# Optimization experiments

Hardware: AMD Instinct MI355X
Metric: run time of the kernel (lower is better)

The kernel has to match this reference:

```python
import jax, jax.numpy as jnp
import numpy as np

NEG_SLOPE = 0.2


def setup_inputs() -> dict:
    key = jax.random.key(0)
    ks = jax.random.split(key, 6)
    N, E, IN, H, D = 50000, 800000, 256, 4, 64
    x = jax.random.normal(ks[0], (N, IN), dtype=jnp.float32)
    edge_index = jax.random.randint(ks[1], (2, E), 0, N, dtype=jnp.int64)
    W = jax.random.normal(ks[2], (IN, H * D), dtype=jnp.float32) / np.sqrt(IN)
    att_src = jax.random.normal(ks[3], (H, D), dtype=jnp.float32) / np.sqrt(D)
    att_dst = jax.random.normal(ks[4], (H, D), dtype=jnp.float32) / np.sqrt(D)
    bias = jnp.zeros((H * D,), dtype=jnp.float32)
    return {"x": x, "edge_index": edge_index, "W": W,
            "att_src": att_src, "att_dst": att_dst, "bias": bias}


def reference(x, edge_index, W, att_src, att_dst, bias):
    N = x.shape[0]
    H, D = att_src.shape
    # add self-loops (PyG GATConv default add_self_loops=True)
    loops = jnp.arange(N, dtype=edge_index.dtype)
    src = jnp.concatenate([edge_index[0], loops])  # [E']
    dst = jnp.concatenate([edge_index[1], loops])  # [E']
    # per-head linear transform: [N, H, D]
    h = (x @ W).reshape(N, H, D)
    # per-node attention logits per head: [N, H]
    a_s = jnp.einsum('nhd,hd->nh', h, att_src)
    a_d = jnp.einsum('nhd,hd->nh', h, att_dst)
    # per-edge raw attention: [E', H]
    e = jax.nn.leaky_relu(a_s[src] + a_d[dst], NEG_SLOPE)
    # softmax over edges grouped by destination node (stable)
    m = jax.ops.segment_max(e, dst, num_segments=N)
    e = jnp.exp(e - m[dst])
    s = jax.ops.segment_sum(e, dst, num_segments=N)
    alpha = e / s[dst]  # every node has a self-loop -> s > 0
    # weighted scatter-aggregate: [N, H, D]
    out = jax.ops.segment_sum(alpha[:, :, None] * h[src], dst, num_segments=N)
    # concat heads + bias; dropout=0.0 -> identity
    return out.reshape(N, H * D) + bias
```

## Files before the change

kernel.cpp:

```cpp
#include <hip/hip_runtime.h>
#include <hip/hip_bf16.h>

#define NEG_SLOPE 0.2f
#define HPAD 264

typedef short short8 __attribute__((ext_vector_type(8)));
typedef float floatx4 __attribute__((ext_vector_type(4)));
typedef unsigned short ushort8v __attribute__((ext_vector_type(8)));
typedef unsigned short ushort4v __attribute__((ext_vector_type(4)));
typedef unsigned int uint4v __attribute__((ext_vector_type(4)));

__device__ __forceinline__ float bf2f_raw(unsigned short u) {
    union { float f; unsigned u; } c; c.u = ((unsigned)u) << 16; return c.f;
}
__device__ __forceinline__ float asf(unsigned u) {
    union { float f; unsigned u; } c; c.u = u; return c.f;
}
__device__ __forceinline__ unsigned short f2bf_raw(float f) {
    union { float f; unsigned u; } c; c.f = f;
    unsigned u = c.u;
    u += 0x7FFFu + ((u >> 16) & 1u);
    return (unsigned short)(u >> 16);
}
__device__ __forceinline__ float ldf(const void* p, size_t i, int f32) {
    return f32 ? ((const float*)p)[i] : bf2f_raw(((const unsigned short*)p)[i]);
}
__device__ __forceinline__ unsigned short ldbf(const void* p, size_t i, int f32) {
    return f32 ? f2bf_raw(((const float*)p)[i]) : ((const unsigned short*)p)[i];
}
__device__ __forceinline__ int clampN(long long v, int N) {
    if (v < 0) v = 0;
    if (v >= N) v = N - 1;
    return (int)v;
}
__device__ __forceinline__ float lrelu(float v) { return v > 0.f ? v : NEG_SLOPE * v; }

__global__ __launch_bounds__(256) void prep_kernel(
    const void* __restrict__ W, unsigned short* __restrict__ Wt,
    const unsigned short* __restrict__ x,
    const unsigned short* __restrict__ as_, const unsigned short* __restrict__ ad_,
    const unsigned* __restrict__ edge_w, int* __restrict__ flags, int edge_words,
    int* __restrict__ deg8, int* __restrict__ bsync, int N8)
{
    __shared__ float sm[256];
    __shared__ unsigned su[256];
    const int t = threadIdx.x;
    const int i = blockIdx.x * 256 + t;

    #pragma unroll
    for (int j = 0; j < 7; ++j) {
        int z = i + j * 65536;
        if (z < N8) deg8[z] = 0;
    }
    if (i < 256) bsync[i] = 0;

    float mw = 0.f;
    for (int k = t; k < 4096; k += 256) {
        float v = fabsf(bf2f_raw(((const unsigned short*)W)[k]));
        mw = fmaxf(mw, (v == v && v < 3e38f) ? v : 1e9f);
    }
    sm[t] = mw; __syncthreads();
    for (int s = 128; s; s >>= 1) { if (t < s) sm[t] = fmaxf(sm[t], sm[t + s]); __syncthreads(); }
    const int wf32 = sm[0] > 100.f;
    __syncthreads();

    if (blockIdx.x == 0) {
        float mx = 0.f, ma = 0.f;
        for (int k = t; k < 4096; k += 256) {
            float v = fabsf(bf2f_raw(x[k]));
            mx = fmaxf(mx, (v == v && v < 3e38f) ? v : 1e9f);
        }
        {
            float v1 = fabsf(bf2f_raw(as_[t]));
            float v2 = fabsf(bf2f_raw(ad_[t]));
            v1 = (v1 == v1 && v1 < 3e38f) ? v1 : 1e9f;
            v2 = (v2 == v2 && v2 < 3e38f) ? v2 : 1e9f;
            ma = fmaxf(v1, v2);
        }
        unsigned ow = 0;
        {
            int k = 2 * t + 1;
            if (k < edge_words) ow = edge_w[k];
        }
        sm[t] = mx; __syncthreads();
        for (int s = 128; s; s >>= 1) { if (t < s) sm[t] = fmaxf(sm[t], sm[t + s]); __syncthreads(); }
        if (t == 0) flags[0] = sm[0] > 100.f;
        __syncthreads();
        sm[t] = ma; __syncthreads();
        for (int s = 128; s; s >>= 1) { if (t < s) sm[t] = fmaxf(sm[t], sm[t + s]); __syncthreads(); }
        if (t == 0) flags[2] = sm[0] > 100.f;
        __syncthreads();
        su[t] = ow; __syncthreads();
        for (int s = 128; s; s >>= 1) { if (t < s) su[t] |= su[t + s]; __syncthreads(); }
        if (t == 0) { flags[3] = (su[0] == 0u); flags[1] = wf32; }
    }

    int j = i & 7;
    int l = (i >> 3) & 63;
    int ks = (i >> 9) & 7;
    int c = i >> 12;
    int k = ks * 32 + (l >> 4) * 8 + j;
    int n = c * 16 + (l & 15);
    Wt[i] = ldbf(W, (size_t)k * 256 + n, wf32);
}

__global__ __launch_bounds__(512) void gemm_count_kernel(
    const void* __restrict__ x, const unsigned short* __restrict__ Wt,
    const void* __restrict__ att_src, const void* __restrict__ att_dst,
    unsigned short* __restrict__ h_out, float* __restrict__ a_s, float* __restrict__ a_d,
    const void* __restrict__ edge, int* __restrict__ deg8, int* __restrict__ rank,
    const int* __restrict__ flags, int N, int E, int ntiles,
    int ngemm, int ncount, int ntotal)
{
    const unsigned long long bi = blockIdx.x;
    const unsigned before = (unsigned)((bi * (unsigned long long)ncount) / ntotal);
    const unsigned after  = (unsigned)(((bi + 1) * (unsigned long long)ncount) / ntotal);

    if (after != before) {
        const int cb = (int)before;
        const int base = cb * 2048 + threadIdx.x * 4;
        if (base >= E) return;
        int* my = deg8 + (size_t)(cb & 7) * N;
        const int cnt = (E - base < 4) ? (E - base) : 4;
        int d[4];
        if (flags[3]) {
            const long long* p = (const long long*)edge + E + base;
            #pragma unroll
            for (int k = 0; k < 4; ++k) d[k] = clampN((k < cnt) ? p[k] : 0, N);
        } else {
            const int* p = (const int*)edge + E + base;
            #pragma unroll
            for (int k = 0; k < 4; ++k) d[k] = clampN((k < cnt) ? (long long)p[k] : 0, N);
        }
        int r[4] = {0, 0, 0, 0};
        #pragma unroll
        for (int k = 0; k < 4; ++k)
            if (k < cnt) r[k] = atomicAdd(&my[d[k]], 1);
        #pragma unroll
        for (int k = 0; k < 4; ++k)
            if (k < cnt) rank[base + k] = r[k];
        return;
    }

    const int gb = (int)(bi - before);

    __shared__ unsigned short sh_h[32][HPAD];
    __shared__ float sh_a[2][32][4];

    const int w = threadIdx.x >> 6;
    const int head = w >> 1;
    const int st = w & 1;
    const int l = threadIdx.x & 63;
    const int lane16 = l & 15;
    const int quad = l >> 4;
    const int xf = flags[0], af = flags[2];
    const int n0w = head * 64;

    float as_att[4], ad_att[4];
    #pragma unroll
    for (int nt = 0; nt < 4; ++nt) {
        as_att[nt] = ldf(att_src, n0w + nt * 16 + lane16, af);
        ad_att[nt] = ldf(att_dst, n0w + nt * 16 + lane16, af);
    }

    for (int tile = gb; tile < ntiles; tile += ngemm) {
        const int m0 = tile * 32;
        int r0 = m0 + st * 16 + lane16;
        if (r0 >= N) r0 = N - 1;

        floatx4 acc[4];
        #pragma unroll
        for (int nt = 0; nt < 4; ++nt) acc[nt] = (floatx4){0.f, 0.f, 0.f, 0.f};

        const unsigned short* wp0 = Wt + (((size_t)head * 32) * 64 + l) * 8;

        #pragma unroll
        for (int half = 0; half < 2; ++half) {
            short8 fa[4];
            if (!xf) {
                const char* b0 = (const char*)x + ((size_t)r0 * 256 + quad * 8) * 2 + half * 256;
                #pragma unroll
                for (int k4 = 0; k4 < 4; ++k4)
                    fa[k4] = *(const short8*)(b0 + k4 * 64);
            } else {
                const float* b0 = (const float*)x + (size_t)r0 * 256 + quad * 8 + half * 128;
                #pragma unroll
                for (int k4 = 0; k4 < 4; ++k4) {
                    #pragma unroll
                    for (int j = 0; j < 8; ++j)
                        fa[k4][j] = (short)f2bf_raw(b0[k4 * 32 + j]);
                }
            }

            #pragma unroll
            for (int k4 = 0; k4 < 4; ++k4) {
                const unsigned short* wp = wp0 + (size_t)(half * 4 + k4) * 512;
                #pragma unroll
                for (int nt = 0; nt < 4; ++nt) {
                    short8 fb = *(const short8*)(wp + nt * 4096);
                    acc[nt] = __builtin_amdgcn_mfma_f32_16x16x32_bf16(fa[k4], fb, acc[nt], 0, 0, 0);
                }
            }
        }

        __syncthreads();

        #pragma unroll
        for (int nt = 0; nt < 4; ++nt) {
            #pragma unroll
            for (int r = 0; r < 4; ++r) {
                sh_h[st * 16 + quad * 4 + r][n0w + nt * 16 + lane16] = f2bf_raw(acc[nt][r]);
            }
        }
        #pragma unroll
        for (int r = 0; r < 4; ++r) {
            float vs = acc[0][r] * as_att[0] + acc[1][r] * as_att[1]
                     + acc[2][r] * as_att[2] + acc[3][r] * as_att[3];
            float vd = acc[0][r] * ad_att[0] + acc[1][r] * ad_att[1]
                     + acc[2][r] * ad_att[2] + acc[3][r] * ad_att[3];
            vs += __shfl_xor(vs, 1); vs += __shfl_xor(vs, 2);
            vs += __shfl_xor(vs, 4); vs += __shfl_xor(vs, 8);
            vd += __shfl_xor(vd, 1); vd += __shfl_xor(vd, 2);
            vd += __shfl_xor(vd, 4); vd += __shfl_xor(vd, 8);
            if (lane16 == 0) {
                const int row = st * 16 + quad * 4 + r;
                sh_a[0][row][head] = vs;
                sh_a[1][row][head] = vd;
            }
        }

        __syncthreads();

        #pragma unroll
        for (int p = 0; p < 2; ++p) {
            const int c = p * 512 + threadIdx.x;
            const int row = c >> 5;
            const int ch = c & 31;
            if (m0 + row < N) {
                ushort8v v = *(const ushort8v*)&sh_h[row][ch * 8];
                *(ushort8v*)(h_out + (size_t)(m0 + row) * 256 + ch * 8) = v;
            }
        }
        {
            const int t = threadIdx.x;
            if (t < 32) {
                if (m0 + t < N)
                    *(floatx4*)&a_s[(size_t)(m0 + t) * 4] = *(const floatx4*)&sh_a[0][t][0];
            } else if (t >= 64 && t < 96) {
                const int r = t - 64;
                if (m0 + r < N)
                    *(floatx4*)&a_d[(size_t)(m0 + r) * 4] = *(const floatx4*)&sh_a[1][r][0];
            }
        }
    }
}

__global__ __launch_bounds__(256) void scan_fused_kernel(
    const int* __restrict__ deg8, int* __restrict__ deg,
    int* __restrict__ row_off, int* __restrict__ cursor8,
    int* __restrict__ bsum, int* __restrict__ bbase, int* __restrict__ bsync,
    int N, int nb)
{
    __shared__ int sh[256];
    __shared__ int is_last;
    __shared__ int sbase;
    const int b = blockIdx.x, t = threadIdx.x;
    const int base_i = b * 1024 + t * 4;
    int v[4], ts = 0;
    #pragma unroll
    for (int i = 0; i < 4; ++i) {
        int idx = base_i + i;
        int tot = 0;
        if (idx < N) {
            #pragma unroll
            for (int x = 0; x < 8; ++x) tot += deg8[(size_t)x * N + idx];
        }
        v[i] = tot;
        ts += tot;
    }
    sh[t] = ts; __syncthreads();
    for (int off = 1; off < 256; off <<= 1) {
        int add = (t >= off) ? sh[t - off] : 0;
        __syncthreads();
        sh[t] += add;
        __syncthreads();
    }
    if (t == 255) {
        __hip_atomic_store(&bsum[b], sh[255], __ATOMIC_RELEASE, __HIP_MEMORY_SCOPE_AGENT);
        int arrived = __hip_atomic_fetch_add(&bsync[0], 1, __ATOMIC_ACQ_REL, __HIP_MEMORY_SCOPE_AGENT);
        is_last = (arrived == nb - 1);
    }
    __syncthreads();
    if (is_last) {
        if (nb <= 64) {
            if (t < 64) {
                int val = (t < nb)
                    ? __hip_atomic_load(&bsum[t], __ATOMIC_ACQUIRE, __HIP_MEMORY_SCOPE_AGENT) : 0;
                int incl = val;
                #pragma unroll
                for (int off = 1; off < 64; off <<= 1) {
                    int u = __shfl_up(incl, off);
                    if (t >= off) incl += u;
                }
                if (t < nb)
                    __hip_atomic_store(&bbase[t], incl - val, __ATOMIC_RELEASE, __HIP_MEMORY_SCOPE_AGENT);
            }
        } else if (t == 0) {
            int run = 0;
            for (int i = 0; i < nb; ++i) {
                int s = __hip_atomic_load(&bsum[i], __ATOMIC_ACQUIRE, __HIP_MEMORY_SCOPE_AGENT);
                __hip_atomic_store(&bbase[i], run, __ATOMIC_RELEASE, __HIP_MEMORY_SCOPE_AGENT);
                run += s;
            }
        }
        __syncthreads();
        if (t == 0)
            __hip_atomic_store(&bsync[1], 1, __ATOMIC_RELEASE, __HIP_MEMORY_SCOPE_AGENT);
    }
    if (t == 0) {
        while (__hip_atomic_load(&bsync[1], __ATOMIC_ACQUIRE, __HIP_MEMORY_SCOPE_AGENT) == 0) {}
        sbase = __hip_atomic_load(&bbase[b], __ATOMIC_RELAXED, __HIP_MEMORY_SCOPE_AGENT);
    }
    __syncthreads();
    int run = sbase + sh[t] - ts;
    #pragma unroll
    for (int i = 0; i < 4; ++i) {
        int idx = base_i + i;
        if (idx < N) {
            row_off[idx] = run;
            deg[idx] = v[i];
            int c = run;
            #pragma unroll
            for (int x = 0; x < 8; ++x) {
                cursor8[(size_t)x * N + idx] = c;
                c += deg8[(size_t)x * N + idx];
            }
        }
        run += v[i];
    }
}

__global__ __launch_bounds__(512) void scatter_kernel(
    const void* __restrict__ edge, const int* __restrict__ cursor8,
    const int* __restrict__ rank, int* __restrict__ elist,
    const int* __restrict__ flags, int E, int N)
{
    const int base = blockIdx.x * 2048 + threadIdx.x * 4;
    if (base >= E) return;
    const int* mybase = cursor8 + (size_t)(blockIdx.x & 7) * N;
    const int cnt = (E - base < 4) ? (E - base) : 4;
    int s[4], d[4];
    if (flags[3]) {
        const long long* ps = (const long long*)edge + base;
        const long long* pd = (const long long*)edge + E + base;
        #pragma unroll
        for (int k = 0; k < 4; ++k) {
            s[k] = clampN((k < cnt) ? ps[k] : 0, N);
            d[k] = clampN((k < cnt) ? pd[k] : 0, N);
        }
    } else {
        const int* ps = (const int*)edge + base;
        const int* pd = (const int*)edge + E + base;
        #pragma unroll
        for (int k = 0; k < 4; ++k) {
            s[k] = clampN((k < cnt) ? (long long)ps[k] : 0, N);
            d[k] = clampN((k < cnt) ? (long long)pd[k] : 0, N);
        }
    }
    #pragma unroll
    for (int k = 0; k < 4; ++k) {
        if (k < cnt) {
            int pos = mybase[d[k]] + rank[base + k];
            elist[pos] = s[k];
        }
    }
}

__global__ __launch_bounds__(256) void aggregate_kernel(
    const int* __restrict__ row_off, const int* __restrict__ deg,
    const int* __restrict__ elist,
    const float* __restrict__ a_s, const float* __restrict__ a_d,
    const unsigned short* __restrict__ h_ws,
    const void* __restrict__ bias, void* __restrict__ out,
    const int* __restrict__ flags, int N)
{
    const int n = blockIdx.x * 4 + (threadIdx.x >> 6);
    if (n >= N) return;
    const int lane = threadIdx.x & 63;
    const int q = lane >> 4;
    const int li = lane & 15;
    const int head = li >> 2;
    const int col0 = li * 16;

    const int dn = deg[n];
    const int row = row_off[n];
    const float adn = a_d[n * 4 + head];
    const float self_logit = lrelu(a_s[n * 4 + head] + adn);

    float acc[16];
    {
        const uint4v* hp = (const uint4v*)(h_ws + (size_t)n * 256 + col0);
        uint4v ha = hp[0], hb = hp[1];
        #pragma unroll
        for (int w = 0; w < 4; ++w) {
            acc[2 * w]         = (q == 0) ? asf(ha[w] << 16) : 0.f;
            acc[2 * w + 1]     = (q == 0) ? asf(ha[w] & 0xffff0000u) : 0.f;
            acc[8 + 2 * w]     = (q == 0) ? asf(hb[w] << 16) : 0.f;
            acc[8 + 2 * w + 1] = (q == 0) ? asf(hb[w] & 0xffff0000u) : 0.f;
        }
    }
    float ssum = (q == 0) ? 1.f : 0.f;

    float asA, asB;
    uint4v hA0, hA1, hB0, hB1;
    int sC, sD;
    {
        int e0 = q, e1 = 4 + q, e2 = 8 + q, e3 = 12 + q;
        int s0 = (e0 < dn) ? elist[row + e0] : n;
        int s1 = (e1 < dn) ? elist[row + e1] : n;
        sC = (e2 < dn) ? elist[row + e2] : n;
        sD = (e3 < dn) ? elist[row + e3] : n;
        asA = a_s[s0 * 4 + head];
        asB = a_s[s1 * 4 + head];
        const uint4v* pA = (const uint4v*)(h_ws + (size_t)s0 * 256 + col0);
        const uint4v* pB = (const uint4v*)(h_ws + (size_t)s1 * 256 + col0);
        hA0 = pA[0]; hA1 = pA[1];
        hB0 = pB[0]; hB1 = pB[1];
    }

    for (int c0 = 0; c0 < dn; c0 += 8) {
        {
            float p = __expf(lrelu(asA + adn) - self_logit);
            p = (c0 + q < dn) ? p : 0.f;
            ssum += p;
            #pragma unroll
            for (int w = 0; w < 4; ++w) {
                acc[2 * w]         += p * asf(hA0[w] << 16);
                acc[2 * w + 1]     += p * asf(hA0[w] & 0xffff0000u);
                acc[8 + 2 * w]     += p * asf(hA1[w] << 16);
                acc[8 + 2 * w + 1] += p * asf(hA1[w] & 0xffff0000u);
            }
        }
        {
            asA = a_s[sC * 4 + head];
            const uint4v* p = (const uint4v*)(h_ws + (size_t)sC * 256 + col0);
            hA0 = p[0]; hA1 = p[1];
            int e = c0 + 16 + q;
            sC = (e < dn) ? elist[row + e] : n;
        }
        {
            float p = __expf(lrelu(asB + adn) - self_logit);
            p = (c0 + 4 + q < dn) ? p : 0.f;
            ssum += p;
            #pragma unroll
            for (int w = 0; w < 4; ++w) {
                acc[2 * w]         += p * asf(hB0[w] << 16);
                acc[2 * w + 1]     += p * asf(hB0[w] & 0xffff0000u);
                acc[8 + 2 * w]     += p * asf(hB1[w] << 16);
                acc[8 + 2 * w + 1] += p * asf(hB1[w] & 0xffff0000u);
            }
        }
        {
            asB = a_s[sD * 4 + head];
            const uint4v* p = (const uint4v*)(h_ws + (size_t)sD * 256 + col0);
            hB0 = p[0]; hB1 = p[1];
            int e = c0 + 20 + q;
            sD = (e < dn) ? elist[row + e] : n;
        }
    }

    #pragma unroll
    for (int j = 0; j < 16; ++j) {
        acc[j] += __shfl_xor(acc[j], 16);
        acc[j] += __shfl_xor(acc[j], 32);
    }
    float stot = ssum + __shfl_xor(ssum, 16);
    stot += __shfl_xor(stot, 32);

    const float inv = 1.f / stot;
    const int j0 = q * 4;
    const int bf32 = flags[2];
    float o[4];
    #pragma unroll
    for (int k = 0; k < 4; ++k)
        o[k] = acc[j0 + k] * inv + ldf(bias, col0 + j0 + k, bf32);
    if (flags[0]) {
        float* op = (float*)out + (size_t)n * 256 + col0 + j0;
        __builtin_nontemporal_store((floatx4){o[0], o[1], o[2], o[3]}, (floatx4*)op);
    } else {
        ushort4v ov;
        #pragma unroll
        for (int k = 0; k < 4; ++k) ov[k] = f2bf_raw(o[k]);
        __builtin_nontemporal_store(ov,
            (ushort4v*)((unsigned short*)out + (size_t)n * 256 + col0 + j0));
    }
}

__global__ __launch_bounds__(256) void sentinel_kernel(unsigned short* out, size_t n, float v) {
    size_t i = (size_t)blockIdx.x * 256 + threadIdx.x;
    if (i < n) out[i] = f2bf_raw(v);
}

extern "C" void kernel_launch(void* const* d_in, const int* in_sizes, int n_in,
                              void* d_out, int out_size, void* d_ws, size_t ws_size,
                              hipStream_t stream) {
    const void* x       = d_in[0];
    const void* edge    = d_in[1];
    const void* W       = d_in[2];
    const void* att_src = d_in[3];
    const void* att_dst = d_in[4];
    const void* bias    = d_in[5];

    const int N = in_sizes[0] / 256;
    const int E = in_sizes[1] / 2;

    char* ws = (char*)d_ws;
    size_t off = 256;
    int*   flags   = (int*)ws;
    float* a_s     = (float*)(ws + off); off += (size_t)N * 4 * sizeof(float);
    float* a_d     = (float*)(ws + off); off += (size_t)N * 4 * sizeof(float);
    int*   deg     = (int*)(ws + off);   off += (size_t)N * sizeof(int);
    int*   row_off = (int*)(ws + off);   off += (size_t)N * sizeof(int);
    int*   bsum    = (int*)(ws + off);   off += 256 * sizeof(int);
    int*   bbase   = (int*)(ws + off);   off += 256 * sizeof(int);
    int*   bsync   = (int*)(ws + off);   off += 256 * sizeof(int);
    unsigned short* Wt = (unsigned short*)(ws + off); off += 65536 * sizeof(unsigned short);
    size_t elist_bytes = (size_t)E * sizeof(int);
    size_t deg8_bytes  = (size_t)8 * N * sizeof(int);
    int*   elist   = (int*)(ws + off);
    int*   deg8    = (int*)(ws + off);   off += (elist_bytes > deg8_bytes ? elist_bytes : deg8_bytes);
    int*   cursor8 = (int*)(ws + off);   off += deg8_bytes;
    int*   rank    = (int*)(ws + off);   off += (size_t)E * sizeof(int);
    unsigned short* h_ws = (unsigned short*)(ws + off);
    const size_t need = off + (size_t)N * 256 * sizeof(unsigned short);

    if (ws_size < need) {
        float v = (float)(ws_size >> 20) * 1000.0f;
        size_t n = (size_t)out_size;
        sentinel_kernel<<<(unsigned)((n + 255) / 256), 256, 0, stream>>>(
            (unsigned short*)d_out, n, v);
        return;
    }

    int edge_words = (2 * E < 512) ? 2 * E : 512;
    prep_kernel<<<256, 256, 0, stream>>>(
        W, Wt, (const unsigned short*)x,
        (const unsigned short*)att_src, (const unsigned short*)att_dst,
        (const unsigned*)edge, flags, edge_words, deg8, bsync, 8 * N);

    const int ntiles = (N + 31) / 32;
    const int ngemm = 1024;
    const int ncount = (E + 2047) / 2048;
    const int ntotal = ngemm + ncount;
    gemm_count_kernel<<<ntotal, 512, 0, stream>>>(
        x, Wt, att_src, att_dst, h_ws, a_s, a_d, edge, deg8, rank,
        flags, N, E, ntiles, ngemm, ncount, ntotal);

    const int nb = (N + 1023) / 1024;
    scan_fused_kernel<<<nb, 256, 0, stream>>>(
        deg8, deg, row_off, cursor8, bsum, bbase, bsync, N, nb);

    scatter_kernel<<<ncount, 512, 0, stream>>>(edge, cursor8, rank, elist, flags, E, N);

    aggregate_kernel<<<(N + 3) / 4, 256, 0, stream>>>(
        row_off, deg, elist, a_s, a_d, h_ws, bias, d_out, flags, N);
}
```

Baseline: 261.1 us.

## Store h in column slabs and split aggregation across slabs per block

The GEMM epilogue now writes h into 8 column slabs of 32 bf16 values each, laid out slab-major. The aggregation kernel launches 8 blocks per node group, each handling one slab, and processes 16 edges concurrently per wave with 4 lanes per edge row. The aim is to shrink per-edge gather width and raise parallelism and locality. In exchange, edge-list, degree and attention-logit loads and the exp computation are repeated once per slab.

```diff
diff --git a/kernel.cpp b/kernel.cpp
--- a/kernel.cpp
+++ b/kernel.cpp
@@ -155,6 +155,7 @@
     const int quad = l >> 4;
     const int xf = flags[0], af = flags[2];
     const int n0w = head * 64;
+    const size_t slabN = (size_t)N * 32;
 
     float as_att[4], ad_att[4];
     #pragma unroll
@@ -234,11 +235,13 @@
         #pragma unroll
         for (int p = 0; p < 2; ++p) {
             const int c = p * 512 + threadIdx.x;
-            const int row = c >> 5;
-            const int ch = c & 31;
+            const int sb = c >> 7;
+            const int inner = c & 127;
+            const int row = inner >> 2;
+            const int c4 = inner & 3;
             if (m0 + row < N) {
-                ushort8v v = *(const ushort8v*)&sh_h[row][ch * 8];
-                *(ushort8v*)(h_out + (size_t)(m0 + row) * 256 + ch * 8) = v;
+                ushort8v v = *(const ushort8v*)&sh_h[row][sb * 32 + c4 * 8];
+                *(ushort8v*)(h_out + (size_t)sb * slabN + (size_t)(m0 + row) * 32 + c4 * 8) = v;
             }
         }
         {
@@ -380,119 +383,90 @@
     const int* __restrict__ row_off, const int* __restrict__ deg,
     const int* __restrict__ elist,
     const float* __restrict__ a_s, const float* __restrict__ a_d,
-    const unsigned short* __restrict__ h_ws,
+    const unsigned short* __restrict__ h_slab,
     const void* __restrict__ bias, void* __restrict__ out,
     const int* __restrict__ flags, int N)
 {
-    const int n = blockIdx.x * 4 + (threadIdx.x >> 6);
+    const int s = blockIdx.x & 7;
+    const int g = blockIdx.x >> 3;
+    const int n = g * 4 + (threadIdx.x >> 6);
     if (n >= N) return;
     const int lane = threadIdx.x & 63;
-    const int q = lane >> 4;
-    const int li = lane & 15;
-    const int head = li >> 2;
-    const int col0 = li * 16;
+    const int slot = lane >> 2;
+    const int sub  = lane & 3;
+    const int head = s >> 1;
+    const size_t slabN = (size_t)N * 32;
+    const unsigned short* hs = h_slab + (size_t)s * slabN;
 
     const int dn = deg[n];
     const int row = row_off[n];
     const float adn = a_d[n * 4 + head];
     const float self_logit = lrelu(a_s[n * 4 + head] + adn);
 
-    float acc[16];
+    float acc[8];
     {
-        const uint4v* hp = (const uint4v*)(h_ws + (size_t)n * 256 + col0);
-        uint4v ha = hp[0], hb = hp[1];
+        const uint4v hv = *(const uint4v*)(hs + (size_t)n * 32 + sub * 8);
         #pragma unroll
         for (int w = 0; w < 4; ++w) {
-            acc[2 * w]         = (q == 0) ? asf(ha[w] << 16) : 0.f;
-            acc[2 * w + 1]     = (q == 0) ? asf(ha[w] & 0xffff0000u) : 0.f;
-            acc[8 + 2 * w]     = (q == 0) ? asf(hb[w] << 16) : 0.f;
-            acc[8 + 2 * w + 1] = (q == 0) ? asf(hb[w] & 0xffff0000u) : 0.f;
-        }
-    }
-    float ssum = (q == 0) ? 1.f : 0.f;
-
-    float asA, asB;
-    uint4v hA0, hA1, hB0, hB1;
-    int sC, sD;
-    {
-        int e0 = q, e1 = 4 + q, e2 = 8 + q, e3 = 12 + q;
-        int s0 = (e0 < dn) ? elist[row + e0] : n;
-        int s1 = (e1 < dn) ? elist[row + e1] : n;
-        sC = (e2 < dn) ? elist[row + e2] : n;
-        sD = (e3 < dn) ? elist[row + e3] : n;
-        asA = a_s[s0 * 4 + head];
-        asB = a_s[s1 * 4 + head];
-        const uint4v* pA = (const uint4v*)(h_ws + (size_t)s0 * 256 + col0);
-        const uint4v* pB = (const uint4v*)(h_ws + (size_t)s1 * 256 + col0);
-        hA0 = pA[0]; hA1 = pA[1];
-        hB0 = pB[0]; hB1 = pB[1];
-    }
-
-    for (int c0 = 0; c0 < dn; c0 += 8) {
-        {
-            float p = __expf(lrelu(asA + adn) - self_logit);
-            p = (c0 + q < dn) ? p : 0.f;
-            ssum += p;
-            #pragma unroll
-            for (int w = 0; w < 4; ++w) {
-                acc[2 * w]         += p * asf(hA0[w] << 16);
-                acc[2 * w + 1]     += p * asf(hA0[w] & 0xffff0000u);
-                acc[8 + 2 * w]     += p * asf(hA1[w] << 16);
-                acc[8 + 2 * w + 1] += p * asf(hA1[w] & 0xffff0000u);
-            }
-        }
-        {
-            asA = a_s[sC * 4 + head];
-            const uint4v* p = (const uint4v*)(h_ws + (size_t)sC * 256 + col0);
-            hA0 = p[0]; hA1 = p[1];
-            int e = c0 + 16 + q;
-            sC = (e < dn) ? elist[row + e] : n;
-        }
-        {
-            float p = __expf(lrelu(asB + adn) - self_logit);
-            p = (c0 + 4 + q < dn) ? p : 0.f;
-            ssum += p;
-            #pragma unroll
-            for (int w = 0; w < 4; ++w) {
-                acc[2 * w]         += p * asf(hB0[w] << 16);
-                acc[2 * w + 1]     += p * asf(hB0[w] & 0xffff0000u);
-                acc[8 + 2 * w]     += p * asf(hB1[w] << 16);
-                acc[8 + 2 * w + 1] += p * asf(hB1[w] & 0xffff0000u);
-            }
-        }
-        {
-            asB = a_s[sD * 4 + head];
-            const uint4v* p = (const uint4v*)(h_ws + (size_t)sD * 256 + col0);
-            hB0 = p[0]; hB1 = p[1];
-            int e = c0 + 20 + q;
-            sD = (e < dn) ? elist[row + e] : n;
-        }
+            acc[2 * w]     = (slot == 0) ? asf(hv[w] << 16) : 0.f;
+            acc[2 * w + 1] = (slot == 0) ? asf(hv[w] & 0xffff0000u) : 0.f;
+        }
+    }
+    float ssum = (slot == 0) ? 1.f : 0.f;
+
+    bool v0 = slot < dn;
+    int s0 = v0 ? elist[row + slot] : n;
+    float as0 = a_s[s0 * 4 + head];
+    uint4v h0 = *(const uint4v*)(hs + (size_t)s0 * 32 + sub * 8);
+
+    for (int c0 = 0; c0 < dn; c0 += 16) {
+        const int e1 = c0 + 16 + slot;
+        const bool v1 = e1 < dn;
+        const int s1 = v1 ? elist[row + e1] : n;
+        const float as1 = a_s[s1 * 4 + head];
+        const uint4v h1 = *(const uint4v*)(hs + (size_t)s1 * 32 + sub * 8);
+
+        float p = v0 ? __expf(lrelu(as0 + adn) - self_logit) : 0.f;
+        ssum += p;
+        #pragma unroll
+        for (int w = 0; w < 4; ++w) {
+            acc[2 * w]     += p * asf(h0[w] << 16);
+            acc[2 * w + 1] += p * asf(h0[w] & 0xffff0000u);
+        }
+        v0 = v1; s0 = s1; as0 = as1; h0 = h1;
     }
 
     #pragma unroll
-    for (int j = 0; j < 16; ++j) {
+    for (int j = 0; j < 8; ++j) {
+        acc[j] += __shfl_xor(acc[j], 4);
+        acc[j] += __shfl_xor(acc[j], 8);
         acc[j] += __shfl_xor(acc[j], 16);
         acc[j] += __shfl_xor(acc[j], 32);
     }
-    float stot = ssum + __shfl_xor(ssum, 16);
-    stot += __shfl_xor(stot, 32);
-
-    const float inv = 1.f / stot;
-    const int j0 = q * 4;
-    const int bf32 = flags[2];
-    float o[4];
-    #pragma unroll
-    for (int k = 0; k < 4; ++k)
-        o[k] = acc[j0 + k] * inv + ldf(bias, col0 + j0 + k, bf32);
-    if (flags[0]) {
-        float* op = (float*)out + (size_t)n * 256 + col0 + j0;
-        __builtin_nontemporal_store((floatx4){o[0], o[1], o[2], o[3]}, (floatx4*)op);
-    } else {
-        ushort4v ov;
-        #pragma unroll
-        for (int k = 0; k < 4; ++k) ov[k] = f2bf_raw(o[k]);
-        __builtin_nontemporal_store(ov,
-            (ushort4v*)((unsigned short*)out + (size_t)n * 256 + col0 + j0));
+    ssum += __shfl_xor(ssum, 4);
+    ssum += __shfl_xor(ssum, 8);
+    ssum += __shfl_xor(ssum, 16);
+    ssum += __shfl_xor(ssum, 32);
+
+    if (slot == 0) {
+        const float inv = 1.f / ssum;
+        const int col0 = s * 32 + sub * 8;
+        const int bf32 = flags[2];
+        float o[8];
+        #pragma unroll
+        for (int k = 0; k < 8; ++k)
+            o[k] = acc[k] * inv + ldf(bias, col0 + k, bf32);
+        if (flags[0]) {
+            float* op = (float*)out + (size_t)n * 256 + col0;
+            __builtin_nontemporal_store((floatx4){o[0], o[1], o[2], o[3]}, (floatx4*)op);
+            __builtin_nontemporal_store((floatx4){o[4], o[5], o[6], o[7]}, (floatx4*)(op + 4));
+        } else {
+            ushort8v ov;
+            #pragma unroll
+            for (int k = 0; k < 8; ++k) ov[k] = f2bf_raw(o[k]);
+            __builtin_nontemporal_store(ov,
+                (ushort8v*)((unsigned short*)out + (size_t)n * 256 + col0));
+        }
     }
 }
 
@@ -562,6 +536,7 @@
 
     scatter_kernel<<<ncount, 512, 0, stream>>>(edge, cursor8, rank, elist, flags, E, N);
 
-    aggregate_kernel<<<(N + 3) / 4, 256, 0, stream>>>(
+    const int agg_blocks = 8 * ((N + 3) / 4);
+    aggregate_kernel<<<agg_blocks, 256, 0, stream>>>(
         row_off, deg, elist, a_s, a_d, h_ws, bias, d_out, flags, N);
 }
```

New measurement: 341.7 us. +30.9%, slower.
